# Kernel tuning notes

Hardware: AMD Instinct MI355X
Metric: run time of the kernel (lower is better)

The kernel has to match this reference:

```python
import math
import jax, jax.numpy as jnp
import numpy as np

D_MODEL = 256
N_HEADS = 8
D_K = D_MODEL // N_HEADS
BS = 2
SEQ = 2048
NEG = -1e32


def _linear(x, W, b):
    return x @ W + b


def _layernorm(x, g, b):
    m = jnp.mean(x, axis=-1, keepdims=True)
    v = jnp.mean((x - m) ** 2, axis=-1, keepdims=True)
    return (x - m) / jnp.sqrt(v + 1e-5) * g + b


def _attention(q, k, v, mask, gammas):
    # q,k,v: [b,h,s,dk]; mask: [1,1,s,s] bool; gammas: [h,1,1]
    d_k = q.shape[-1]
    scores = jnp.einsum('bhqd,bhkd->bhqk', q, k) / math.sqrt(d_k)
    S = scores.shape[-1]
    # distance-decay bias (computed under stop_gradient, as torch.no_grad + detach)
    sm = jax.lax.stop_gradient(jax.nn.softmax(jnp.where(mask, scores, NEG), axis=-1))
    distcum = jnp.cumsum(sm, axis=-1)
    disttot = jnp.sum(sm, axis=-1, keepdims=True)
    idx = jnp.arange(S, dtype=scores.dtype)
    pos = jnp.abs(idx[None, :] - idx[:, None])[None, None]  # |i-j|
    dist = jax.lax.stop_gradient(
        jnp.sqrt(jnp.clip((disttot - distcum) * pos, 0.0, None)))
    gamma = -jax.nn.softplus(gammas)[None]  # [1,h,1,1]
    eff = jnp.clip(jnp.exp(dist * gamma), 1e-5, 1e5)
    scores = jnp.where(mask, scores * eff, NEG)
    scores = jnp.where(mask, jax.nn.softmax(scores, axis=-1), 0.0)
    return jnp.einsum('bhqk,bhkd->bhqd', scores, v)


def _mha(qx, kx, vx, Wq, bq, Wk, bk, Wv, bv, Wo, bo, gammas, mask):
    bs = qx.shape[0]
    def split(x, W, b):
        return _linear(x, W, b).reshape(bs, -1, N_HEADS, D_K).transpose(0, 2, 1, 3)
    q = split(qx, Wq, bq)
    k = split(kx, Wk, bk)
    v = split(vx, Wv, bv)
    o = _attention(q, k, v, mask, gammas)
    o = o.transpose(0, 2, 1, 3).reshape(bs, -1, D_MODEL)
    return _linear(o, Wo, bo)


def _layer(query, key, values, Wq, bq, Wk, bk, Wv, bv, Wo, bo, gammas, ln_g, ln_b, peek_cur):
    S = query.shape[1]
    mask = jnp.tril(jnp.ones((S, S), dtype=bool), 0 if peek_cur else -1)[None, None]
    out = _mha(query, key, values, Wq, bq, Wk, bk, Wv, bv, Wo, bo, gammas, mask)
    return _layernorm(query + out, ln_g, ln_b)


def _forward(q_emb, qa_emb,
             b1_Wq, b1_bq, b1_Wv, b1_bv, b1_Wo, b1_bo, b1_gam, b1_lng, b1_lnb,
             b2_Wq, b2_bq, b2_Wv, b2_bv, b2_Wo, b2_bo, b2_gam, b2_lng, b2_lnb,
             b3_Wq, b3_bq, b3_Wk, b3_bk, b3_Wv, b3_bv, b3_Wo, b3_bo, b3_gam, b3_lng, b3_lnb,
             know_params, lk_W, lk_b, lv_W, lv_b):
    # blocks 1 & 2: kq_same -> k projection shares q projection weights
    hq = _layer(q_emb, q_emb, q_emb,
                b1_Wq, b1_bq, b1_Wq, b1_bq, b1_Wv, b1_bv, b1_Wo, b1_bo,
                b1_gam, b1_lng, b1_lnb, peek_cur=True)
    ha = _layer(qa_emb, qa_emb, qa_emb,
                b2_Wq, b2_bq, b2_Wq, b2_bq, b2_Wv, b2_bv, b2_Wo, b2_bo,
                b2_gam, b2_lng, b2_lnb, peek_cur=True)
    query = jnp.broadcast_to(know_params, hq.shape)
    h = _layer(query, hq, ha,
               b3_Wq, b3_bq, b3_Wk, b3_bk, b3_Wv, b3_bv, b3_Wo, b3_bo,
               b3_gam, b3_lng, b3_lnb, peek_cur=False)
    bs, S, d = hq.shape
    key = jax.nn.sigmoid(_linear(
        jnp.broadcast_to(know_params, (bs, S, d)).reshape(bs, S, N_HEADS, D_K),
        lk_W, lk_b)).reshape(bs * S, N_HEADS, d)
    value = jax.nn.sigmoid(_linear(
        h.reshape(bs, S, N_HEADS, D_K), lv_W, lv_b)).reshape(bs * S, N_HEADS, d)
    beta = jnp.einsum('nhd,nd->nh', key, q_emb.reshape(bs * S, d))
    alpha = jax.nn.softmax(beta, axis=-1)
    h = jnp.einsum('nh,nhd->nd', alpha, value).reshape(bs, S, d)
    return h


def setup_inputs() -> dict:
    keys = iter(jax.random.split(jax.random.key(0), 64))
    def nrm(shape, scale=0.02):
        return jax.random.normal(next(keys), shape, dtype=jnp.float32) * scale
    def uni(shape):
        return jax.random.uniform(next(keys), shape, dtype=jnp.float32, minval=-1.0, maxval=1.0)
    d = D_MODEL
    inp = {
        'q_emb': nrm((BS, SEQ, d), 1.0),
        'qa_emb': nrm((BS, SEQ, d), 1.0),
    }
    for blk in ('b1', 'b2'):
        inp[blk + '_Wq'] = nrm((d, d)); inp[blk + '_bq'] = jnp.zeros((d,), jnp.float32)
        inp[blk + '_Wv'] = nrm((d, d)); inp[blk + '_bv'] = jnp.zeros((d,), jnp.float32)
        inp[blk + '_Wo'] = nrm((d, d)); inp[blk + '_bo'] = jnp.zeros((d,), jnp.float32)
        inp[blk + '_gam'] = uni((N_HEADS, 1, 1))
        inp[blk + '_lng'] = jnp.ones((d,), jnp.float32)
        inp[blk + '_lnb'] = jnp.zeros((d,), jnp.float32)
    inp['b3_Wq'] = nrm((d, d)); inp['b3_bq'] = jnp.zeros((d,), jnp.float32)
    inp['b3_Wk'] = nrm((d, d)); inp['b3_bk'] = jnp.zeros((d,), jnp.float32)
    inp['b3_Wv'] = nrm((d, d)); inp['b3_bv'] = jnp.zeros((d,), jnp.float32)
    inp['b3_Wo'] = nrm((d, d)); inp['b3_bo'] = jnp.zeros((d,), jnp.float32)
    inp['b3_gam'] = uni((N_HEADS, 1, 1))
    inp['b3_lng'] = jnp.ones((d,), jnp.float32)
    inp['b3_lnb'] = jnp.zeros((d,), jnp.float32)
    inp['know_params'] = uni((1, 1, d))
    inp['lk_W'] = nrm((D_K, d)); inp['lk_b'] = jnp.zeros((d,), jnp.float32)
    inp['lv_W'] = nrm((D_K, d)); inp['lv_b'] = jnp.zeros((d,), jnp.float32)
    return inp


def reference(q_emb, qa_emb,
              b1_Wq, b1_bq, b1_Wv, b1_bv, b1_Wo, b1_bo, b1_gam, b1_lng, b1_lnb,
              b2_Wq, b2_bq, b2_Wv, b2_bv, b2_Wo, b2_bo, b2_gam, b2_lng, b2_lnb,
              b3_Wq, b3_bq, b3_Wk, b3_bk, b3_Wv, b3_bv, b3_Wo, b3_bo, b3_gam, b3_lng, b3_lnb,
              know_params, lk_W, lk_b, lv_W, lv_b):
    return _forward(q_emb, qa_emb,
                    b1_Wq, b1_bq, b1_Wv, b1_bv, b1_Wo, b1_bo, b1_gam, b1_lng, b1_lnb,
                    b2_Wq, b2_bq, b2_Wv, b2_bv, b2_Wo, b2_bo, b2_gam, b2_lng, b2_lnb,
                    b3_Wq, b3_bq, b3_Wk, b3_bk, b3_Wv, b3_bv, b3_Wo, b3_bo, b3_gam, b3_lng, b3_lnb,
                    know_params, lk_W, lk_b, lv_W, lv_b)
```

## Files before the change

### kernel.cpp

```cpp
#include <hip/hip_runtime.h>
#include <hip/hip_bf16.h>

#define DM 256
#define NH 8
#define DK 32
#define BSZ 2
#define SEQ 2048
#define ROWS (BSZ*SEQ)
#define RT 16
#define SRB 2312
#define SRBH 1144

static __device__ __forceinline__ int sw8(int j) { return j + ((j >> 6) << 3); }

typedef __attribute__((ext_vector_type(8))) short short8;
typedef __attribute__((ext_vector_type(4))) float f32x4;

static __device__ __forceinline__ unsigned short f2bf(float f) {
    unsigned u = __float_as_uint(f);
    return (unsigned short)((u + 0x7FFFu + ((u >> 16) & 1u)) >> 16);
}
static __device__ __forceinline__ float bf2f(unsigned short h) {
    return __uint_as_float(((unsigned)h) << 16);
}

static __device__ __forceinline__ unsigned cvtpk(float lo, float hi) {
    unsigned r;
    asm("v_cvt_pk_bf16_f32 %0, %1, %2" : "=v"(r) : "v"(lo), "v"(hi));
    return r;
}

static __device__ __forceinline__ float ex2(float x) { return __builtin_amdgcn_exp2f(x); }
static __device__ __forceinline__ float sqt(float x) { return __builtin_amdgcn_sqrtf(x); }
static __device__ __forceinline__ float rcp(float x) { return __builtin_amdgcn_rcpf(x); }

template<int CTRL, int RM>
static __device__ __forceinline__ float dppadd(float x) {
    int s = __builtin_amdgcn_update_dpp(0, __float_as_int(x), CTRL, RM, 0xf, true);
    return x + __int_as_float(s);
}
static __device__ __forceinline__ float scan32(float x) {
    x = dppadd<0x111, 0xf>(x);
    x = dppadd<0x112, 0xf>(x);
    x = dppadd<0x114, 0xf>(x);
    x = dppadd<0x118, 0xf>(x);
    x = dppadd<0x142, 0xa>(x);
    return x;
}
static __device__ __forceinline__ float red16(float x) {
    x = dppadd<0x0B1, 0xf>(x);
    x = dppadd<0x04E, 0xf>(x);
    x = dppadd<0x124, 0xf>(x);
    x = dppadd<0x128, 0xf>(x);
    return x;
}
static __device__ __forceinline__ float bcast31(float x) {
    return __int_as_float(__builtin_amdgcn_ds_swizzle(__float_as_int(x), 0x03E0));
}
static __device__ __forceinline__ float swz_x16(float x) {
    return __int_as_float(__builtin_amdgcn_ds_swizzle(__float_as_int(x), 0x401F));
}

static __device__ __forceinline__ void unpack4(uint2 u, float& s0, float& s1,
                                               float& s2, float& s3) {
    s0 = __uint_as_float(u.x << 16);
    s1 = __uint_as_float(u.x & 0xFFFF0000u);
    s2 = __uint_as_float(u.y << 16);
    s3 = __uint_as_float(u.y & 0xFFFF0000u);
}

static __device__ __forceinline__ uint2 decay_quad(
    float s0, float s1, float s2, float s3v,
    float e0, float e1, float e2, float e3,
    float cum, float pq, float linv,
    float l, float gamma2, float& l2)
{
    float p0, p1, p2, p3;
    cum += e0;
    { float dist = sqt(fmaxf((l - cum) * pq, 0.f));
      float eff = fmaxf(ex2(dist * gamma2), 1e-5f);
      p0 = ex2(s0 * eff); l2 += p0; }
    cum += e1;
    { float dist = sqt(fmaxf((l - cum) * (pq - linv), 0.f));
      float eff = fmaxf(ex2(dist * gamma2), 1e-5f);
      p1 = ex2(s1 * eff); l2 += p1; }
    cum += e2;
    { float dist = sqt(fmaxf((l - cum) * (pq - 2.f * linv), 0.f));
      float eff = fmaxf(ex2(dist * gamma2), 1e-5f);
      p2 = ex2(s2 * eff); l2 += p2; }
    cum += e3;
    { float dist = sqt(fmaxf((l - cum) * (pq - 3.f * linv), 0.f));
      float eff = fmaxf(ex2(dist * gamma2), 1e-5f);
      p3 = ex2(s3v * eff); l2 += p3; }
    uint2 st;
    st.x = cvtpk(p0, p1);
    st.y = cvtpk(p2, p3);
    return st;
}

#define MFMA_BF16 __builtin_amdgcn_mfma_f32_16x16x32_bf16
#define LOG2E 1.44269504088896340736f

static __device__ __forceinline__ float waveRedSum(float v) {
    #pragma unroll
    for (int off = 32; off > 0; off >>= 1) v += __shfl_down(v, off, 64);
    return v;
}

__global__ __launch_bounds__(256) void convert_w_kernel(
    const float* __restrict__ S0, const float* __restrict__ S1, const float* __restrict__ S2,
    const float* __restrict__ S3, const float* __restrict__ S4, const float* __restrict__ S5,
    const float* __restrict__ S6, const float* __restrict__ S7, const float* __restrict__ S8,
    unsigned short* __restrict__ dst,
    const float* __restrict__ know,
    const float* __restrict__ W3q, const float* __restrict__ b3q,
    const float* __restrict__ lkW, const float* __restrict__ lkb,
    float* __restrict__ q3row, float* __restrict__ key8)
{
    __shared__ float kn[DM];
    int s = blockIdx.y;
    if (s == 9) {
        if (blockIdx.x != 0) return;
        int t = threadIdx.x;
        kn[t] = know[t];
        __syncthreads();
        float acc = b3q[t];
        for (int c = 0; c < DM; ++c) acc += kn[c] * W3q[(size_t)c * DM + t];
        q3row[t] = acc;
        float bk = lkb[t];
        for (int h = 0; h < NH; ++h) {
            float a = bk;
            #pragma unroll
            for (int c = 0; c < DK; ++c) a += kn[h * DK + c] * lkW[(size_t)c * DM + t];
            key8[(size_t)h * DM + t] = 1.f / (1.f + __expf(-a));
        }
        return;
    }
    const float* W;
    if (s == 0) W = S0; else if (s == 1) W = S1; else if (s == 2) W = S2;
    else if (s == 3) W = S3; else if (s == 4) W = S4; else if (s == 5) W = S5;
    else if (s == 6) W = S6; else if (s == 7) W = S7; else W = S8;
    unsigned short* H = dst + (size_t)s * 131072;
    unsigned short* L = H + 65536;

    int e = blockIdx.x * 1024 + threadIdx.x * 4;
    int k = e >> 8, n = e & 255;
    float4 w4 = *(const float4*)(W + e);
    float v[4] = {w4.x, w4.y, w4.z, w4.w};
    #pragma unroll
    for (int i = 0; i < 4; ++i) {
        unsigned short h = f2bf(v[i]);
        H[(size_t)(n + i) * 256 + k] = h;
        L[(size_t)(n + i) * 256 + k] = (unsigned short)f2bf(v[i] - bf2f(h));
    }
}

__global__ __launch_bounds__(256) void gemm4_kernel(
    const float* __restrict__ X0, const unsigned short* __restrict__ H0, const float* __restrict__ B0,
    float* __restrict__ Y0, unsigned short* __restrict__ K0o, unsigned short* __restrict__ V0o,
    const float* __restrict__ X1, const unsigned short* __restrict__ H1, const float* __restrict__ B1,
    float* __restrict__ Y1, unsigned short* __restrict__ K1o, unsigned short* __restrict__ V1o,
    const float* __restrict__ X2, const unsigned short* __restrict__ H2, const float* __restrict__ B2,
    float* __restrict__ Y2, unsigned short* __restrict__ K2o, unsigned short* __restrict__ V2o,
    const float* __restrict__ X3, const unsigned short* __restrict__ H3, const float* __restrict__ B3,
    float* __restrict__ Y3, unsigned short* __restrict__ K3o, unsigned short* __restrict__ V3o)
{
    const float *X, *Bias; const unsigned short* H; float* Yf;
    unsigned short *KSo, *VSo;
    int s = blockIdx.y;
    if (s == 0)      { X = X0; H = H0; Bias = B0; Yf = Y0; KSo = K0o; VSo = V0o; }
    else if (s == 1) { X = X1; H = H1; Bias = B1; Yf = Y1; KSo = K1o; VSo = V1o; }
    else if (s == 2) { X = X2; H = H2; Bias = B2; Yf = Y2; KSo = K2o; VSo = V2o; }
    else             { X = X3; H = H3; Bias = B3; Yf = Y3; KSo = K3o; VSo = V3o; }
    const unsigned short* L = H + 65536;

    __shared__ __align__(16) unsigned short XhL[16 * 264];
    __shared__ __align__(16) unsigned short XlL[16 * 264];
    __shared__ __align__(16) unsigned short vt[256][24];
    int t = threadIdx.x;
    int r0 = blockIdx.x * 16;
    {
        int r = t >> 4, c0 = (t & 15) * 16;
        const float* xp = X + (size_t)(r0 + r) * DM + c0;
        #pragma unroll
        for (int i = 0; i < 16; i += 4) {
            float4 v4 = *(const float4*)(xp + i);
            float vv[4] = {v4.x, v4.y, v4.z, v4.w};
            #pragma unroll
            for (int j = 0; j < 4; ++j) {
                unsigned short h = f2bf(vv[j]);
                XhL[r * 264 + c0 + i + j] = h;
                XlL[r * 264 + c0 + i + j] = (unsigned short)f2bf(vv[j] - bf2f(h));
            }
        }
    }
    __syncthreads();
    int lane = t & 63, wv = t >> 6;
    int m = lane & 15, quad = lane >> 4;
    f32x4 aa[4];
    #pragma unroll
    for (int nt = 0; nt < 4; ++nt) { aa[nt][0]=0.f; aa[nt][1]=0.f; aa[nt][2]=0.f; aa[nt][3]=0.f; }
    #pragma unroll 1
    for (int kc = 0; kc < 8; ++kc) {
        int k0 = kc * 32;
        short8 Ah = *(const short8*)&XhL[m * 264 + k0 + quad * 8];
        short8 Al = *(const short8*)&XlL[m * 264 + k0 + quad * 8];
        size_t boff = (size_t)(wv * 64 + m) * 256 + k0 + quad * 8;
        #pragma unroll
        for (int nt = 0; nt < 4; ++nt) {
            short8 Bh = *(const short8*)(H + boff + nt * 16 * 256);
            short8 Bl = *(const short8*)(L + boff + nt * 16 * 256);
            aa[nt] = MFMA_BF16(Al, Bh, aa[nt], 0, 0, 0);
            aa[nt] = MFMA_BF16(Ah, Bl, aa[nt], 0, 0, 0);
            aa[nt] = MFMA_BF16(Ah, Bh, aa[nt], 0, 0, 0);
        }
    }
    int col0 = wv * 64 + m;
    #pragma unroll
    for (int nt = 0; nt < 4; ++nt) {
        int col = col0 + nt * 16;
        float bb = Bias[col];
        float yv[4];
        #pragma unroll
        for (int g = 0; g < 4; ++g) yv[g] = aa[nt][g] + bb;
        if (Yf) {
            #pragma unroll
            for (int g = 0; g < 4; ++g)
                Yf[(size_t)(r0 + quad * 4 + g) * DM + col] = yv[g];
        }
        if (KSo) {
            unsigned short* KH = KSo;
            unsigned short* KL = KSo + (size_t)ROWS * DM;
            #pragma unroll
            for (int g = 0; g < 4; ++g) {
                unsigned short hb = f2bf(yv[g]);
                KH[(size_t)(r0 + quad * 4 + g) * DM + col] = hb;
                KL[(size_t)(r0 + quad * 4 + g) * DM + col] =
                    (unsigned short)f2bf(yv[g] - bf2f(hb));
            }
        }
        if (VSo) {
            ushort4 h4;
            h4.x = f2bf(yv[0]); h4.y = f2bf(yv[1]);
            h4.z = f2bf(yv[2]); h4.w = f2bf(yv[3]);
            *(ushort4*)&vt[col][quad * 4] = h4;
        }
    }
    if (VSo) {
        __syncthreads();
        short8 v0 = *(const short8*)&vt[t][0];
        short8 v1 = *(const short8*)&vt[t][8];
        unsigned short* vp = VSo + (size_t)t * ROWS + r0;
        *(short8*)vp = v0;
        *(short8*)(vp + 8) = v1;
    }
}

__global__ __launch_bounds__(256) void gemm_ln2_kernel(
    const float* __restrict__ X0, const unsigned short* __restrict__ H0, const float* __restrict__ B0,
    const float* __restrict__ R0, const float* __restrict__ G0, const float* __restrict__ L0,
    float* __restrict__ Y0, int bc0,
    const float* __restrict__ X1, const unsigned short* __restrict__ H1, const float* __restrict__ B1,
    const float* __restrict__ R1, const float* __restrict__ G1, const float* __restrict__ L1,
    float* __restrict__ Y1, int bc1)
{
    const float *X, *Bias, *R, *G, *Lb; const unsigned short* H; float* Y; int bc;
    if (blockIdx.y == 0) { X=X0; H=H0; Bias=B0; R=R0; G=G0; Lb=L0; Y=Y0; bc=bc0; }
    else                 { X=X1; H=H1; Bias=B1; R=R1; G=G1; Lb=L1; Y=Y1; bc=bc1; }
    const unsigned short* L = H + 65536;

    __shared__ __align__(16) unsigned short XhL[16 * 264];
    __shared__ __align__(16) unsigned short XlL[16 * 264];
    __shared__ __align__(16) float yl[16 * 260];
    int t = threadIdx.x;
    int r0 = blockIdx.x * 16;
    {   int r = t >> 4, c0 = (t & 15) * 16;
        const float* xp = X + (size_t)(r0 + r) * DM + c0;
        #pragma unroll
        for (int i = 0; i < 16; i += 4) {
            float4 v4 = *(const float4*)(xp + i);
            float vv[4] = {v4.x, v4.y, v4.z, v4.w};
            #pragma unroll
            for (int j = 0; j < 4; ++j) {
                unsigned short h = f2bf(vv[j]);
                XhL[r * 264 + c0 + i + j] = h;
                XlL[r * 264 + c0 + i + j] = (unsigned short)f2bf(vv[j] - bf2f(h));
            }
        }
    }
    __syncthreads();
    int lane = t & 63, wv = t >> 6;
    int m = lane & 15, quad = lane >> 4;
    f32x4 aa[4];
    #pragma unroll
    for (int nt = 0; nt < 4; ++nt) { aa[nt][0]=0.f; aa[nt][1]=0.f; aa[nt][2]=0.f; aa[nt][3]=0.f; }
    #pragma unroll 1
    for (int kc = 0; kc < 8; ++kc) {
        int k0 = kc * 32;
        short8 Ah = *(const short8*)&XhL[m * 264 + k0 + quad * 8];
        short8 Al = *(const short8*)&XlL[m * 264 + k0 + quad * 8];
        size_t boff = (size_t)(wv * 64 + m) * 256 + k0 + quad * 8;
        #pragma unroll
        for (int nt = 0; nt < 4; ++nt) {
            short8 Bh = *(const short8*)(H + boff + nt * 16 * 256);
            short8 Bl = *(const short8*)(L + boff + nt * 16 * 256);
            aa[nt] = MFMA_BF16(Al, Bh, aa[nt], 0, 0, 0);
            aa[nt] = MFMA_BF16(Ah, Bl, aa[nt], 0, 0, 0);
            aa[nt] = MFMA_BF16(Ah, Bh, aa[nt], 0, 0, 0);
        }
    }
    {
        int col0 = wv * 64 + m;
        #pragma unroll
        for (int nt = 0; nt < 4; ++nt) {
            int col = col0 + nt * 16;
            float bb = Bias[col];
            #pragma unroll
            for (int g = 0; g < 4; ++g) {
                int row = quad * 4 + g;
                float res = bc ? R[col] : R[(size_t)(r0 + row) * DM + col];
                yl[row * 260 + col] = aa[nt][g] + bb + res;
            }
        }
    }
    __syncthreads();
    {
        int r = t >> 4, c0 = (t & 15) * 16;
        float vals[16];
        float part = 0.f;
        #pragma unroll
        for (int i = 0; i < 16; ++i) { vals[i] = yl[r * 260 + c0 + i]; part += vals[i]; }
        #pragma unroll
        for (int off = 8; off; off >>= 1) part += __shfl_xor(part, off, 16);
        float mean = part * (1.f / DM);
        float vp = 0.f;
        #pragma unroll
        for (int i = 0; i < 16; ++i) { float d = vals[i] - mean; vp += d * d; }
        #pragma unroll
        for (int off = 8; off; off >>= 1) vp += __shfl_xor(vp, off, 16);
        float rs = rsqrtf(vp * (1.f / DM) + 1e-5f);
        float* yp = Y + (size_t)(r0 + r) * DM + c0;
        #pragma unroll
        for (int i = 0; i < 16; i += 4) {
            float4 o;
            o.x = (vals[i+0] - mean) * rs * G[c0+i+0] + Lb[c0+i+0];
            o.y = (vals[i+1] - mean) * rs * G[c0+i+1] + Lb[c0+i+1];
            o.z = (vals[i+2] - mean) * rs * G[c0+i+2] + Lb[c0+i+2];
            o.w = (vals[i+3] - mean) * rs * G[c0+i+3] + Lb[c0+i+3];
            *(float4*)(yp + i) = o;
        }
    }
}

__global__ __launch_bounds__(256) void score3a_kernel(
    const float* __restrict__ q3row, const float* __restrict__ K3,
    unsigned short* __restrict__ S3, float* __restrict__ C3,
    float* __restrict__ Csum)
{
    __shared__ float wsum[4];
    int s = blockIdx.x;
    int bh = blockIdx.y;
    int b = bh >> 3, h = bh & 7;
    int t = threadIdx.x;
    int lane = t & 63, wv = t >> 6;
    int j = s * 256 + t;
    const float scaleL2 = 0.17677669529663687f * LOG2E;
    float qv[DK];
    #pragma unroll
    for (int d = 0; d < DK; d += 4) {
        float4 qq = *(const float4*)(q3row + h * DK + d);
        qv[d+0] = qq.x * scaleL2; qv[d+1] = qq.y * scaleL2;
        qv[d+2] = qq.z * scaleL2; qv[d+3] = qq.w * scaleL2;
    }
    const float* kp = K3 + ((size_t)b * SEQ + j) * DM + h * DK;
    float kv[DK];
    #pragma unroll
    for (int d = 0; d < DK; d += 4) {
        float4 kq = *(const float4*)(kp + d);
        kv[d+0] = kq.x; kv[d+1] = kq.y; kv[d+2] = kq.z; kv[d+3] = kq.w;
    }
    float sc = 0.f;
    #pragma unroll
    for (int d = 0; d < DK; ++d) sc += qv[d] * kv[d];
    unsigned short sb16 = f2bf(sc);
    float e = ex2(bf2f(sb16));
    float x = e;
    #pragma unroll
    for (int off = 1; off < 64; off <<= 1) {
        float y = __shfl_up(x, off, 64);
        if (lane >= off) x += y;
    }
    if (lane == 63) wsum[wv] = x;
    __syncthreads();
    float woff = 0.f;
    for (int w = 0; w < wv; ++w) woff += wsum[w];
    float inc = woff + x;
    S3[(size_t)bh * SEQ + j] = sb16;
    C3[(size_t)bh * SEQ + j] = inc;
    if (t == 255) Csum[bh * 8 + s] = inc;
}

__global__ __launch_bounds__(256) void score3b_kernel(
    const float* __restrict__ Csum, float* __restrict__ C3)
{
    int s = blockIdx.x + 1;
    int bh = blockIdx.y;
    int t = threadIdx.x;
    float off = 0.f;
    for (int w = 0; w < s; ++w) off += Csum[bh * 8 + w];
    C3[(size_t)bh * SEQ + s * 256 + t] += off;
}

__global__ __launch_bounds__(512) void attn12_kernel(
    const float* __restrict__ Q0,
    const unsigned short* __restrict__ KS0, const unsigned short* __restrict__ VS0,
    const float* __restrict__ g0, float* __restrict__ O0,
    const float* __restrict__ Q1,
    const unsigned short* __restrict__ KS1, const unsigned short* __restrict__ VS1,
    const float* __restrict__ g1, float* __restrict__ O1)
{
    __shared__ __align__(16) unsigned short SB[RT * SRB];
    __shared__ float qs[RT][DK];
    __shared__ float l2inv_s[RT];
    __shared__ float rowsum[8 * RT];

    int bx, by;
    {
        int flat = (int)blockIdx.y * 128 + (int)blockIdx.x;
        int per = (32 * 128) >> 3;
        int nf = (flat & 7) * per + (flat >> 3);
        by = nf >> 7;
        bx = nf & 127;
    }
    int set = by >> 4, bh = by & 15;
    const float* Q = set ? Q1 : Q0;
    const unsigned short* KS = set ? KS1 : KS0;
    const unsigned short* VS = set ? VS1 : VS0;
    const float* gm = set ? g1 : g0;
    float* O = set ? O1 : O0;

    int b = bh >> 3, h = bh & 7;
    int i0 = (127 - bx) * RT;
    int t = threadIdx.x;
    size_t base = ((size_t)b * SEQ) * DM + (size_t)h * DK;

    int njAll = i0 + RT;
    int njPad32 = (njAll + 31) & ~31;
    int njPad128 = (njAll + 127) & ~127;
    const float scaleL2 = 0.17677669529663687f * LOG2E;

    {
        int r = t >> 5, d = t & 31;
        qs[r][d] = Q[base + (size_t)(i0 + r) * DM + d];
    }
    __syncthreads();

    {
        int wave = t >> 6, lane = t & 63;
        int m = lane & 15, quad = lane >> 4;

        float av[8];
        {
            float4 qa = *(const float4*)&qs[m][8 * quad];
            float4 qb = *(const float4*)&qs[m][8 * quad + 4];
            av[0]=qa.x*scaleL2; av[1]=qa.y*scaleL2; av[2]=qa.z*scaleL2; av[3]=qa.w*scaleL2;
            av[4]=qb.x*scaleL2; av[5]=qb.y*scaleL2; av[6]=qb.z*scaleL2; av[7]=qb.w*scaleL2;
        }
        short8 Ah;
        #pragma unroll
        for (int i = 0; i < 8; ++i) Ah[i] = (short)f2bf(av[i]);

        const unsigned short* KH = KS;
        const unsigned short* KL = KS + (size_t)ROWS * DM;
        size_t rowb = (size_t)b * SEQ;
        int njr0 = i0 + quad * 4 + 1;
        float rp0 = 0.f, rp1 = 0.f, rp2 = 0.f, rp3 = 0.f;
        int nChunks = (njAll + 15) >> 4;
        #pragma unroll 2
        for (int c = wave; c < nChunks; c += 8) {
            int j0 = c << 4;
            size_t off = (rowb + j0 + m) * DM + h * DK + quad * 8;
            short8 Bh = *(const short8*)&KH[off];
            short8 Bl = *(const short8*)&KL[off];
            f32x4 acc = {0.f, 0.f, 0.f, 0.f};
            acc = MFMA_BF16(Ah, Bl, acc, 0, 0, 0);
            acc = MFMA_BF16(Ah, Bh, acc, 0, 0, 0);
            int jcol = j0 + m;
            int sj = sw8(jcol);
            unsigned pk01 = cvtpk(acc[0], acc[1]);
            unsigned pk23 = cvtpk(acc[2], acc[3]);
            SB[(quad * 4 + 0) * SRB + sj] = (unsigned short)pk01;
            SB[(quad * 4 + 1) * SRB + sj] = (unsigned short)(pk01 >> 16);
            SB[(quad * 4 + 2) * SRB + sj] = (unsigned short)pk23;
            SB[(quad * 4 + 3) * SRB + sj] = (unsigned short)(pk23 >> 16);
            rp0 += (jcol < njr0 + 0) ? ex2(acc[0]) : 0.f;
            rp1 += (jcol < njr0 + 1) ? ex2(acc[1]) : 0.f;
            rp2 += (jcol < njr0 + 2) ? ex2(acc[2]) : 0.f;
            rp3 += (jcol < njr0 + 3) ? ex2(acc[3]) : 0.f;
        }
        rp0 = red16(rp0); rp1 = red16(rp1);
        rp2 = red16(rp2); rp3 = red16(rp3);
        if (m == 0) {
            rowsum[wave * RT + quad * 4 + 0] = rp0;
            rowsum[wave * RT + quad * 4 + 1] = rp1;
            rowsum[wave * RT + quad * 4 + 2] = rp2;
            rowsum[wave * RT + quad * 4 + 3] = rp3;
        }
    }
    __syncthreads();

    {
        int r = t >> 5, c = t & 31;
        int nj = i0 + r + 1;
        for (int j = nj + c; j < njPad128; j += 32)
            SB[r * SRB + sw8(j)] = 0xFF80u;
    }
    __syncthreads();

    {
        int r = t >> 5, c = t & 31;
        int i = i0 + r;
        unsigned short* Sr = SB + r * SRB;
        float gamma2 = -log1pf(__expf(gm[h])) * LOG2E;

        float l = 0.f;
        #pragma unroll
        for (int w = 0; w < 8; ++w) l += rowsum[w * RT + r];
        float linv = rcp(l);

        float l2 = 0.f;
        float Bc = 0.f;
        int nIter = (njPad32 + 127) >> 7;
        int pairs = nIter >> 1;
        uint2 nxA, nxB;
        nxA = *(const uint2*)&Sr[sw8(4 * c)];
        nxB = *(const uint2*)&Sr[sw8(4 * c + 128)];
        #pragma unroll 1
        for (int k = 0; k < pairs; ++k) {
            int j4a = 256 * k + 4 * c;
            int j4b = j4a + 128;
            uint2 uA = nxA;
            uint2 uB = nxB;
            nxA = *(const uint2*)&Sr[sw8(j4a + 256)];
            nxB = *(const uint2*)&Sr[sw8(j4b + 256)];
            float a0, a1, a2, a3, b0, b1, b2, b3;
            unpack4(uA, a0, a1, a2, a3);
            unpack4(uB, b0, b1, b2, b3);
            float eA0 = ex2(a0), eA1 = ex2(a1), eA2 = ex2(a2), eA3 = ex2(a3);
            float eB0 = ex2(b0), eB1 = ex2(b1), eB2 = ex2(b2), eB3 = ex2(b3);
            float sigA = eA0 + eA1 + eA2 + eA3;
            float sigB = eB0 + eB1 + eB2 + eB3;
            float xA = scan32(sigA);
            float xB = scan32(sigB);
            float totA = bcast31(xA);
            float totB = bcast31(xB);
            float cumA = Bc + (xA - sigA);
            float cumB = Bc + totA + (xB - sigB);
            Bc += totA + totB;
            float pqA = (float)(i - j4a) * linv;
            float pqB = pqA - 128.f * linv;
            uint2 stA = decay_quad(a0, a1, a2, a3, eA0, eA1, eA2, eA3,
                                   cumA, pqA, linv, l, gamma2, l2);
            uint2 stB = decay_quad(b0, b1, b2, b3, eB0, eB1, eB2, eB3,
                                   cumB, pqB, linv, l, gamma2, l2);
            *(uint2*)&Sr[sw8(j4a)] = stA;
            *(uint2*)&Sr[sw8(j4b)] = stB;
        }
        if (nIter & 1) {
            int j4a = 256 * pairs + 4 * c;
            uint2 uA = nxA;
            float a0, a1, a2, a3;
            unpack4(uA, a0, a1, a2, a3);
            float eA0 = ex2(a0), eA1 = ex2(a1), eA2 = ex2(a2), eA3 = ex2(a3);
            float sigA = eA0 + eA1 + eA2 + eA3;
            float xA = scan32(sigA);
            float cumA = Bc + (xA - sigA);
            float pqA = (float)(i - j4a) * linv;
            uint2 stA = decay_quad(a0, a1, a2, a3, eA0, eA1, eA2, eA3,
                                   cumA, pqA, linv, l, gamma2, l2);
            *(uint2*)&Sr[sw8(j4a)] = stA;
        }
        l2 = red16(l2);
        l2 += swz_x16(l2);
        if (c == 0) l2inv_s[r] = rcp(l2);
    }
    __syncthreads();

    {
        int wave = t >> 6, lane = t & 63;
        int n16 = lane & 15, quad = lane >> 4;
        const unsigned short* VH = VS;
        size_t vb0 = (size_t)(h * DK + n16) * ROWS + (size_t)b * SEQ;
        size_t vb1 = (size_t)(h * DK + 16 + n16) * ROWS + (size_t)b * SEQ;
        f32x4 oc0 = {0.f,0.f,0.f,0.f}, oc1 = {0.f,0.f,0.f,0.f};
        #pragma unroll 2
        for (int j0 = wave * 32; j0 < njPad32; j0 += 256) {
            short8 Ap = *(const short8*)&SB[n16 * SRB + sw8(j0 + quad * 8)];
            int jo = j0 + quad * 8;
            short8 Bh0 = *(const short8*)&VH[vb0 + jo];
            short8 Bh1 = *(const short8*)&VH[vb1 + jo];
            oc0 = MFMA_BF16(Ap, Bh0, oc0, 0, 0, 0);
            oc1 = MFMA_BF16(Ap, Bh1, oc1, 0, 0, 0);
        }
        __syncthreads();
        float* FS = (float*)SB;
        #pragma unroll
        for (int g = 0; g < 4; ++g) {
            int row = quad * 4 + g;
            FS[wave * 512 + row * 32 + n16] = oc0[g];
            FS[wave * 512 + row * 32 + 16 + n16] = oc1[g];
        }
    }
    __syncthreads();
    {
        float* FS = (float*)SB;
        int r2 = t >> 5, d = t & 31;
        float sum = 0.f;
        #pragma unroll
        for (int w = 0; w < 8; ++w)
            sum += FS[w * 512 + r2 * 32 + d];
        O[base + (size_t)(i0 + r2) * DM + d] = sum * l2inv_s[r2];
    }
}

__global__ __launch_bounds__(512) void attn3_kernel(
    const unsigned short* __restrict__ VS, const float* __restrict__ gm8,
    float* __restrict__ O,
    const unsigned short* __restrict__ S3g, const float* __restrict__ C3g)
{
    __shared__ __align__(16) unsigned short SBH[RT * SRBH];
    __shared__ float l2inv_s[RT];

    int bx, by;
    {
        int flat = (int)blockIdx.y * 128 + (int)blockIdx.x;
        int per = (16 * 128) >> 3;
        int nf = (flat & 7) * per + (flat >> 3);
        by = nf >> 7;
        bx = nf & 127;
    }
    int bh = by;
    int b = bh >> 3, h = bh & 7;
    int i0 = (127 - bx) * RT;
    int t = threadIdx.x;
    size_t base = ((size_t)b * SEQ) * DM + (size_t)h * DK;

    int njAll = i0 + RT - 1;
    int njPad32 = (njAll + 31) & ~31;
    int E = ((njPad32 + 127) >> 7) << 7;

    int r = t >> 5, c = t & 31;
    int i = i0 + r;
    int nj = i;
    unsigned short* Sr = SBH + r * SRBH;
    float gamma2 = -log1pf(__expf(gm8[h])) * LOG2E;
    const unsigned short* s3p = S3g + (size_t)bh * SEQ;
    const float* c3p = C3g + (size_t)bh * SEQ;
    float Lc = (nj > 0) ? c3p[nj - 1] : 0.f;
    float linv = (nj > 0) ? rcp(Lc) : 0.f;
    float li2 = linv + linv, li3 = li2 + linv;
    float l2 = 0.f;

    int wave = t >> 6, lane = t & 63;
    int n16 = lane & 15, quad = lane >> 4;
    size_t rowb = (size_t)b * SEQ;
    size_t vb0 = (size_t)(h * DK + n16) * ROWS + rowb;
    size_t vb1 = (size_t)(h * DK + 16 + n16) * ROWS + rowb;
    f32x4 oc0 = {0.f,0.f,0.f,0.f}, oc1 = {0.f,0.f,0.f,0.f};

    #pragma unroll 1
    for (int hbase = 0; hbase < E; hbase += 1024) {
        int hend = min(hbase + 1024, E);
        #pragma unroll 1
        for (int j4 = hbase + 4 * c; j4 < hend; j4 += 128) {
            uint2 su = *(const uint2*)&s3p[j4];
            float4 C4 = *(const float4*)&c3p[j4];
            float s0 = __uint_as_float(su.x << 16);
            float s1 = __uint_as_float(su.x & 0xFFFF0000u);
            float s2 = __uint_as_float(su.y << 16);
            float s3v = __uint_as_float(su.y & 0xFFFF0000u);
            float pq = (float)(i - j4) * linv;
            float p0, p1, p2, p3;
            { float dist = sqt(fmaxf((Lc - C4.x) * pq, 0.f));
              float eff = fmaxf(ex2(dist * gamma2), 1e-5f);
              p0 = (j4 + 0 < nj) ? ex2(s0 * eff) : 0.f; l2 += p0; }
            { float dist = sqt(fmaxf((Lc - C4.y) * (pq - linv), 0.f));
              float eff = fmaxf(ex2(dist * gamma2), 1e-5f);
              p1 = (j4 + 1 < nj) ? ex2(s1 * eff) : 0.f; l2 += p1; }
            { float dist = sqt(fmaxf((Lc - C4.z) * (pq - li2), 0.f));
              float eff = fmaxf(ex2(dist * gamma2), 1e-5f);
              p2 = (j4 + 2 < nj) ? ex2(s2 * eff) : 0.f; l2 += p2; }
            { float dist = sqt(fmaxf((Lc - C4.w) * (pq - li3), 0.f));
              float eff = fmaxf(ex2(dist * gamma2), 1e-5f);
              p3 = (j4 + 3 < nj) ? ex2(s3v * eff) : 0.f; l2 += p3; }
            uint2 st;
            st.x = cvtpk(p0, p1);
            st.y = cvtpk(p2, p3);
            *(uint2*)&Sr[sw8(j4 - hbase)] = st;
        }
        __syncthreads();
        int pend = min(hbase + 1024, njPad32);
        #pragma unroll 1
        for (int j0 = hbase + wave * 32; j0 < pend; j0 += 256) {
            short8 Ap = *(const short8*)&SBH[n16 * SRBH + sw8(j0 - hbase + quad * 8)];
            int jo = j0 + quad * 8;
            short8 Bh0 = *(const short8*)&VS[vb0 + jo];
            short8 Bh1 = *(const short8*)&VS[vb1 + jo];
            oc0 = MFMA_BF16(Ap, Bh0, oc0, 0, 0, 0);
            oc1 = MFMA_BF16(Ap, Bh1, oc1, 0, 0, 0);
        }
        __syncthreads();
    }

    l2 = red16(l2);
    l2 += swz_x16(l2);
    if (c == 0) l2inv_s[r] = (nj > 0) ? rcp(l2) : 0.f;
    float* FS = (float*)SBH;
    #pragma unroll
    for (int g = 0; g < 4; ++g) {
        int row = quad * 4 + g;
        FS[wave * 512 + row * 32 + n16] = oc0[g];
        FS[wave * 512 + row * 32 + 16 + n16] = oc1[g];
    }
    __syncthreads();
    {
        int r2 = t >> 5, d = t & 31;
        float sum = 0.f;
        #pragma unroll
        for (int w = 0; w < 8; ++w)
            sum += FS[w * 512 + r2 * 32 + d];
        O[base + (size_t)(i0 + r2) * DM + d] = sum * l2inv_s[r2];
    }
}

__global__ __launch_bounds__(256) void readout_kernel(
    const float* __restrict__ h3, const float* __restrict__ qe,
    const float* __restrict__ key8,
    const float* __restrict__ lvW, const float* __restrict__ lvb,
    float* __restrict__ out)
{
    __shared__ float hrow[DM], qrow[DM];
    __shared__ float red8[4][NH];
    int n = blockIdx.x, t = threadIdx.x;
    int lane = t & 63, wid = t >> 6;
    hrow[t] = h3[(size_t)n * DM + t];
    qrow[t] = qe[(size_t)n * DM + t];
    __syncthreads();
    float ph[NH];
    #pragma unroll
    for (int h = 0; h < NH; ++h) {
        float v = key8[(size_t)h * DM + t] * qrow[t];
        v = waveRedSum(v);
        ph[h] = v;
    }
    if (lane == 0) {
        #pragma unroll
        for (int h = 0; h < NH; ++h) red8[wid][h] = ph[h];
    }
    __syncthreads();
    float beta[NH];
    #pragma unroll
    for (int h = 0; h < NH; ++h)
        beta[h] = red8[0][h] + red8[1][h] + red8[2][h] + red8[3][h];
    float bv = lvb[t];
    float vh[NH];
    for (int h = 0; h < NH; ++h) {
        float a = bv;
        #pragma unroll
        for (int c = 0; c < DK; ++c) a += hrow[h * DK + c] * lvW[(size_t)c * DM + t];
        vh[h] = 1.f / (1.f + __expf(-a));
    }
    float mb = beta[0];
    #pragma unroll
    for (int h = 1; h < NH; ++h) mb = fmaxf(mb, beta[h]);
    float se = 0.f, eh[NH];
    #pragma unroll
    for (int h = 0; h < NH; ++h) { eh[h] = __expf(beta[h] - mb); se += eh[h]; }
    float sinv = 1.f / se;
    float o = 0.f;
    #pragma unroll
    for (int h = 0; h < NH; ++h) o += eh[h] * sinv * vh[h];
    out[(size_t)n * DM + t] = o;
}

extern "C" void kernel_launch(void* const* d_in, const int* in_sizes, int n_in,
                              void* d_out, int out_size, void* d_ws, size_t ws_size,
                              hipStream_t stream) {
    (void)in_sizes; (void)n_in; (void)out_size; (void)ws_size;
    const float* q_emb  = (const float*)d_in[0];
    const float* qa_emb = (const float*)d_in[1];
    const float* b1_Wq = (const float*)d_in[2];
    const float* b1_bq = (const float*)d_in[3];
    const float* b1_Wv = (const float*)d_in[4];
    const float* b1_bv = (const float*)d_in[5];
    const float* b1_Wo = (const float*)d_in[6];
    const float* b1_bo = (const float*)d_in[7];
    const float* b1_gam = (const float*)d_in[8];
    const float* b1_lng = (const float*)d_in[9];
    const float* b1_lnb = (const float*)d_in[10];
    const float* b2_Wq = (const float*)d_in[11];
    const float* b2_bq = (const float*)d_in[12];
    const float* b2_Wv = (const float*)d_in[13];
    const float* b2_bv = (const float*)d_in[14];
    const float* b2_Wo = (const float*)d_in[15];
    const float* b2_bo = (const float*)d_in[16];
    const float* b2_gam = (const float*)d_in[17];
    const float* b2_lng = (const float*)d_in[18];
    const float* b2_lnb = (const float*)d_in[19];
    const float* b3_Wq = (const float*)d_in[20];
    const float* b3_bq = (const float*)d_in[21];
    const float* b3_Wk = (const float*)d_in[22];
    const float* b3_bk = (const float*)d_in[23];
    const float* b3_Wv = (const float*)d_in[24];
    const float* b3_bv = (const float*)d_in[25];
    const float* b3_Wo = (const float*)d_in[26];
    const float* b3_bo = (const float*)d_in[27];
    const float* b3_gam = (const float*)d_in[28];
    const float* b3_lng = (const float*)d_in[29];
    const float* b3_lnb = (const float*)d_in[30];
    const float* know  = (const float*)d_in[31];
    const float* lk_W  = (const float*)d_in[32];
    const float* lk_b  = (const float*)d_in[33];
    const float* lv_W  = (const float*)d_in[34];
    const float* lv_b  = (const float*)d_in[35];

    const size_t SLAB = (size_t)ROWS * DM;
    const size_t USLAB = 2 * SLAB;
    float* A1 = (float*)d_ws;
    float* A2 = A1 + SLAB;
    float* C1 = A2 + SLAB;
    float* C2 = C1 + SLAB;
    unsigned short* KS1 = (unsigned short*)(C2 + SLAB);
    unsigned short* KS2 = KS1 + USLAB;
    unsigned short* VS1 = KS2 + USLAB;
    unsigned short* VS2 = VS1 + USLAB;
    float* q3row = (float*)(VS2 + USLAB);
    float* key8  = q3row + DM;
    unsigned short* Wsp = (unsigned short*)(key8 + NH * DM);
    unsigned short* S3buf = Wsp + (size_t)9 * 131072;
    float* C3buf = (float*)(S3buf + 16 * SEQ);
    float* Csum  = C3buf + 16 * SEQ;
    float* hq = (float*)KS1;
    float* ha = (float*)KS2;
    float* k3 = A1;
    unsigned short* VS3 = VS1;
    float* O3 = C1;
    float* h3 = C2;

    auto WH = [&](int i) { return Wsp + (size_t)i * 131072; };

    dim3 blk(256);
    dim3 ablk(512);
    dim3 agrid2(SEQ / RT, 32);
    dim3 agrid1(SEQ / RT, 16);
    dim3 rgrid(ROWS);

    convert_w_kernel<<<dim3(64, 10), blk, 0, stream>>>(
        b1_Wq, b1_Wv, b1_Wo, b2_Wq, b2_Wv, b2_Wo, b3_Wk, b3_Wv, b3_Wo, Wsp,
        know, b3_Wq, b3_bq, lk_W, lk_b, q3row, key8);

    gemm4_kernel<<<dim3(ROWS/16, 4), blk, 0, stream>>>(
        q_emb,  WH(0), b1_bq, A1,      KS1,     nullptr,
        q_emb,  WH(1), b1_bv, nullptr, nullptr, VS1,
        qa_emb, WH(3), b2_bq, A2,      KS2,     nullptr,
        qa_emb, WH(4), b2_bv, nullptr, nullptr, VS2);

    attn12_kernel<<<agrid2, ablk, 0, stream>>>(
        A1, KS1, VS1, b1_gam, C1,
        A2, KS2, VS2, b2_gam, C2);

    gemm_ln2_kernel<<<dim3(ROWS/16, 2), blk, 0, stream>>>(
        C1, WH(2), b1_bo, q_emb,  b1_lng, b1_lnb, hq, 0,
        C2, WH(5), b2_bo, qa_emb, b2_lng, b2_lnb, ha, 0);

    gemm4_kernel<<<dim3(ROWS/16, 2), blk, 0, stream>>>(
        hq, WH(6), b3_bk, k3,      nullptr, nullptr,
        ha, WH(7), b3_bv, nullptr, nullptr, VS3,
        hq, WH(6), b3_bk, k3,      nullptr, nullptr,
        hq, WH(6), b3_bk, k3,      nullptr, nullptr);

    score3a_kernel<<<dim3(8, 16), blk, 0, stream>>>(q3row, k3, S3buf, C3buf, Csum);
    score3b_kernel<<<dim3(7, 16), blk, 0, stream>>>(Csum, C3buf);

    attn3_kernel<<<agrid1, ablk, 0, stream>>>(VS3, b3_gam, O3, S3buf, C3buf);

    gemm_ln2_kernel<<<dim3(ROWS/16, 1), blk, 0, stream>>>(
        O3, WH(8), b3_bo, know, b3_lng, b3_lnb, h3, 1,
        O3, WH(8), b3_bo, know, b3_lng, b3_lnb, h3, 1);

    readout_kernel<<<rgrid, blk, 0, stream>>>(h3, q_emb, key8, lv_W, lv_b,
                                              (float*)d_out);
}
```

Baseline: 425.3 us.

## Keep attention scores in registers and compute decay per chunk in attn12

Restructures the attn12 kernel so each wave keeps its bf16 QK scores in registers instead of writing them all to shared memory. Per-32-column block exp-sums are stored in a small LDS table and prefix-scanned, and each wave then computes the distance-decay probabilities for its own chunks with an in-wave 16-lane scan. The probabilities are written to a half-size LDS buffer in two 1024-column phases and fed straight into the PV MFMA. This cuts shared-memory footprint and LDS round-trips and removes the separate per-row scan pass, at the cost of many more live registers (32 packed score registers per thread) and extra barriers.

Result: slower. 440.8 us (+3.6%).

```diff
diff --git a/kernel.cpp b/kernel.cpp
--- a/kernel.cpp
+++ b/kernel.cpp
@@ -8,8 +8,8 @@
 #define SEQ 2048
 #define ROWS (BSZ*SEQ)
 #define RT 16
-#define SRB 2312
 #define SRBH 1144
+#define SRBW 1160
 
 static __device__ __forceinline__ int sw8(int j) { return j + ((j >> 6) << 3); }
 
@@ -47,6 +47,13 @@
     x = dppadd<0x142, 0xa>(x);
     return x;
 }
+static __device__ __forceinline__ float scan16(float x) {
+    x = dppadd<0x111, 0xf>(x);
+    x = dppadd<0x112, 0xf>(x);
+    x = dppadd<0x114, 0xf>(x);
+    x = dppadd<0x118, 0xf>(x);
+    return x;
+}
 static __device__ __forceinline__ float red16(float x) {
     x = dppadd<0x0B1, 0xf>(x);
     x = dppadd<0x04E, 0xf>(x);
@@ -57,45 +64,11 @@
 static __device__ __forceinline__ float bcast31(float x) {
     return __int_as_float(__builtin_amdgcn_ds_swizzle(__float_as_int(x), 0x03E0));
 }
+static __device__ __forceinline__ float bcast15(float x) {
+    return __int_as_float(__builtin_amdgcn_ds_swizzle(__float_as_int(x), 0x01F0));
+}
 static __device__ __forceinline__ float swz_x16(float x) {
     return __int_as_float(__builtin_amdgcn_ds_swizzle(__float_as_int(x), 0x401F));
-}
-
-static __device__ __forceinline__ void unpack4(uint2 u, float& s0, float& s1,
-                                               float& s2, float& s3) {
-    s0 = __uint_as_float(u.x << 16);
-    s1 = __uint_as_float(u.x & 0xFFFF0000u);
-    s2 = __uint_as_float(u.y << 16);
-    s3 = __uint_as_float(u.y & 0xFFFF0000u);
-}
-
-static __device__ __forceinline__ uint2 decay_quad(
-    float s0, float s1, float s2, float s3v,
-    float e0, float e1, float e2, float e3,
-    float cum, float pq, float linv,
-    float l, float gamma2, float& l2)
-{
-    float p0, p1, p2, p3;
-    cum += e0;
-    { float dist = sqt(fmaxf((l - cum) * pq, 0.f));
-      float eff = fmaxf(ex2(dist * gamma2), 1e-5f);
-      p0 = ex2(s0 * eff); l2 += p0; }
-    cum += e1;
-    { float dist = sqt(fmaxf((l - cum) * (pq - linv), 0.f));
-      float eff = fmaxf(ex2(dist * gamma2), 1e-5f);
-      p1 = ex2(s1 * eff); l2 += p1; }
-    cum += e2;
-    { float dist = sqt(fmaxf((l - cum) * (pq - 2.f * linv), 0.f));
-      float eff = fmaxf(ex2(dist * gamma2), 1e-5f);
-      p2 = ex2(s2 * eff); l2 += p2; }
-    cum += e3;
-    { float dist = sqt(fmaxf((l - cum) * (pq - 3.f * linv), 0.f));
-      float eff = fmaxf(ex2(dist * gamma2), 1e-5f);
-      p3 = ex2(s3v * eff); l2 += p3; }
-    uint2 st;
-    st.x = cvtpk(p0, p1);
-    st.y = cvtpk(p2, p3);
-    return st;
 }
 
 #define MFMA_BF16 __builtin_amdgcn_mfma_f32_16x16x32_bf16
@@ -419,10 +392,10 @@
     const unsigned short* __restrict__ KS1, const unsigned short* __restrict__ VS1,
     const float* __restrict__ g1, float* __restrict__ O1)
 {
-    __shared__ __align__(16) unsigned short SB[RT * SRB];
-    __shared__ float qs[RT][DK];
-    __shared__ float l2inv_s[RT];
-    __shared__ float rowsum[8 * RT];
+    __shared__ __align__(16) unsigned short PB[RT * SRBW];
+    __shared__ float ct[16 * 64];
+    __shared__ float l_s[16];
+    __shared__ float wl2[8][16];
 
     int bx, by;
     {
@@ -442,184 +415,194 @@
     int b = bh >> 3, h = bh & 7;
     int i0 = (127 - bx) * RT;
     int t = threadIdx.x;
+    int wave = t >> 6, lane = t & 63;
+    int m = lane & 15, quad = lane >> 4;
     size_t base = ((size_t)b * SEQ) * DM + (size_t)h * DK;
+    size_t rowb = (size_t)b * SEQ;
 
     int njAll = i0 + RT;
-    int njPad32 = (njAll + 31) & ~31;
-    int njPad128 = (njAll + 127) & ~127;
+    int nChunks = njAll >> 4;
+    int nb32 = (nChunks + 1) >> 1;
+    int njPad32 = nb32 << 5;
+
     const float scaleL2 = 0.17677669529663687f * LOG2E;
 
+    short8 Ah;
     {
-        int r = t >> 5, d = t & 31;
-        qs[r][d] = Q[base + (size_t)(i0 + r) * DM + d];
+        const float* qp = Q + base + (size_t)(i0 + m) * DM + quad * 8;
+        float4 qa = *(const float4*)qp;
+        float4 qb = *(const float4*)(qp + 4);
+        float av[8] = {qa.x, qa.y, qa.z, qa.w, qb.x, qb.y, qb.z, qb.w};
+        #pragma unroll
+        for (int i = 0; i < 8; ++i) Ah[i] = (short)f2bf(av[i] * scaleL2);
+    }
+
+    const unsigned short* KH = KS;
+    const unsigned short* KL = KS + (size_t)ROWS * DM;
+    int njr[4];
+    #pragma unroll
+    for (int g = 0; g < 4; ++g) njr[g] = i0 + quad * 4 + g + 1;
+
+    unsigned spk[32];
+
+    #pragma unroll
+    for (int bb = 0; bb < 8; ++bb) {
+        int blk = wave + bb * 8;
+        if (blk < nb32) {
+            float ctv[4] = {0.f, 0.f, 0.f, 0.f};
+            #pragma unroll
+            for (int half = 0; half < 2; ++half) {
+                int c = blk * 2 + half;
+                if (c < nChunks) {
+                    int j0 = c << 4;
+                    size_t off = (rowb + j0 + m) * DM + h * DK + quad * 8;
+                    short8 Bh = *(const short8*)&KH[off];
+                    short8 Bl = *(const short8*)&KL[off];
+                    f32x4 acc = {0.f, 0.f, 0.f, 0.f};
+                    acc = MFMA_BF16(Ah, Bl, acc, 0, 0, 0);
+                    acc = MFMA_BF16(Ah, Bh, acc, 0, 0, 0);
+                    int jcol = j0 + m;
+                    unsigned short u0 = f2bf(acc[0]), u1 = f2bf(acc[1]);
+                    unsigned short u2 = f2bf(acc[2]), u3 = f2bf(acc[3]);
+                    spk[bb * 4 + half * 2 + 0] = (unsigned)u0 | ((unsigned)u1 << 16);
+                    spk[bb * 4 + half * 2 + 1] = (unsigned)u2 | ((unsigned)u3 << 16);
+                    ctv[0] += (jcol < njr[0]) ? ex2(bf2f(u0)) : 0.f;
+                    ctv[1] += (jcol < njr[1]) ? ex2(bf2f(u1)) : 0.f;
+                    ctv[2] += (jcol < njr[2]) ? ex2(bf2f(u2)) : 0.f;
+                    ctv[3] += (jcol < njr[3]) ? ex2(bf2f(u3)) : 0.f;
+                }
+            }
+            #pragma unroll
+            for (int g = 0; g < 4; ++g) ctv[g] = red16(ctv[g]);
+            if (m == 0) {
+                #pragma unroll
+                for (int g = 0; g < 4; ++g) ct[(quad * 4 + g) * 64 + blk] = ctv[g];
+            }
+        }
     }
     __syncthreads();
 
     {
-        int wave = t >> 6, lane = t & 63;
-        int m = lane & 15, quad = lane >> 4;
-
-        float av[8];
-        {
-            float4 qa = *(const float4*)&qs[m][8 * quad];
-            float4 qb = *(const float4*)&qs[m][8 * quad + 4];
-            av[0]=qa.x*scaleL2; av[1]=qa.y*scaleL2; av[2]=qa.z*scaleL2; av[3]=qa.w*scaleL2;
-            av[4]=qb.x*scaleL2; av[5]=qb.y*scaleL2; av[6]=qb.z*scaleL2; av[7]=qb.w*scaleL2;
-        }
-        short8 Ah;
-        #pragma unroll
-        for (int i = 0; i < 8; ++i) Ah[i] = (short)f2bf(av[i]);
-
-        const unsigned short* KH = KS;
-        const unsigned short* KL = KS + (size_t)ROWS * DM;
-        size_t rowb = (size_t)b * SEQ;
-        int njr0 = i0 + quad * 4 + 1;
-        float rp0 = 0.f, rp1 = 0.f, rp2 = 0.f, rp3 = 0.f;
-        int nChunks = (njAll + 15) >> 4;
-        #pragma unroll 2
-        for (int c = wave; c < nChunks; c += 8) {
-            int j0 = c << 4;
-            size_t off = (rowb + j0 + m) * DM + h * DK + quad * 8;
-            short8 Bh = *(const short8*)&KH[off];
-            short8 Bl = *(const short8*)&KL[off];
-            f32x4 acc = {0.f, 0.f, 0.f, 0.f};
-            acc = MFMA_BF16(Ah, Bl, acc, 0, 0, 0);
-            acc = MFMA_BF16(Ah, Bh, acc, 0, 0, 0);
-            int jcol = j0 + m;
-            int sj = sw8(jcol);
-            unsigned pk01 = cvtpk(acc[0], acc[1]);
-            unsigned pk23 = cvtpk(acc[2], acc[3]);
-            SB[(quad * 4 + 0) * SRB + sj] = (unsigned short)pk01;
-            SB[(quad * 4 + 1) * SRB + sj] = (unsigned short)(pk01 >> 16);
-            SB[(quad * 4 + 2) * SRB + sj] = (unsigned short)pk23;
-            SB[(quad * 4 + 3) * SRB + sj] = (unsigned short)(pk23 >> 16);
-            rp0 += (jcol < njr0 + 0) ? ex2(acc[0]) : 0.f;
-            rp1 += (jcol < njr0 + 1) ? ex2(acc[1]) : 0.f;
-            rp2 += (jcol < njr0 + 2) ? ex2(acc[2]) : 0.f;
-            rp3 += (jcol < njr0 + 3) ? ex2(acc[3]) : 0.f;
-        }
-        rp0 = red16(rp0); rp1 = red16(rp1);
-        rp2 = red16(rp2); rp3 = red16(rp3);
-        if (m == 0) {
-            rowsum[wave * RT + quad * 4 + 0] = rp0;
-            rowsum[wave * RT + quad * 4 + 1] = rp1;
-            rowsum[wave * RT + quad * 4 + 2] = rp2;
-            rowsum[wave * RT + quad * 4 + 3] = rp3;
-        }
-    }
-    __syncthreads();
-
+        int r = t >> 5, c0 = t & 31;
+        float v0 = (2 * c0     < nb32) ? ct[r * 64 + 2 * c0]     : 0.f;
+        float v1 = (2 * c0 + 1 < nb32) ? ct[r * 64 + 2 * c0 + 1] : 0.f;
+        float loc = v0 + v1;
+        float x = scan32(loc);
+        float tot = bcast31(x);
+        float excl = x - loc;
+        float2 pr; pr.x = excl; pr.y = excl + v0;
+        *(float2*)&ct[r * 64 + 2 * c0] = pr;
+        if (c0 == 0) l_s[r] = tot;
+    }
+    __syncthreads();
+
+    float gamma2 = -log1pf(__expf(gm[h])) * LOG2E;
+    float linv[4], rowc[4], l2[4];
+    #pragma unroll
+    for (int g = 0; g < 4; ++g) {
+        linv[g] = rcp(l_s[quad * 4 + g]);
+        rowc[g] = (float)(i0 + quad * 4 + g - m);
+        l2[g] = 0.f;
+    }
+
+    size_t vb0 = (size_t)(h * DK + m) * ROWS + rowb;
+    size_t vb1 = vb0 + (size_t)16 * ROWS;
+    f32x4 oc0 = {0.f,0.f,0.f,0.f}, oc1 = {0.f,0.f,0.f,0.f};
+
+    #pragma unroll
+    for (int q = 0; q < 2; ++q) {
+        if (q * 1024 < njPad32) {
+            #pragma unroll
+            for (int j = 0; j < 4; ++j) {
+                int bb = q * 4 + j;
+                int blk = wave + bb * 8;
+                if (blk < nb32) {
+                    float pre[4];
+                    #pragma unroll
+                    for (int g = 0; g < 4; ++g) pre[g] = ct[(quad * 4 + g) * 64 + blk];
+                    #pragma unroll
+                    for (int half = 0; half < 2; ++half) {
+                        int c = blk * 2 + half;
+                        int j0 = c << 4;
+                        int lc0 = j0 - q * 1024;
+                        int sbase = lc0 + ((lc0 >> 6) << 3);
+                        unsigned short* Srow = PB + sbase + m;
+                        if (c < nChunks) {
+                            int jcol = j0 + m;
+                            unsigned pk0 = spk[bb * 4 + half * 2 + 0];
+                            unsigned pk1 = spk[bb * 4 + half * 2 + 1];
+                            float s[4];
+                            s[0] = bf2f((unsigned short)pk0);
+                            s[1] = bf2f((unsigned short)(pk0 >> 16));
+                            s[2] = bf2f((unsigned short)pk1);
+                            s[3] = bf2f((unsigned short)(pk1 >> 16));
+                            float x[4];
+                            #pragma unroll
+                            for (int g = 0; g < 4; ++g)
+                                x[g] = (jcol < njr[g]) ? ex2(s[g]) : 0.f;
+                            #pragma unroll
+                            for (int g = 0; g < 4; ++g) x[g] = scan16(x[g]);
+                            #pragma unroll
+                            for (int g = 0; g < 4; ++g) {
+                                float cum = pre[g] + x[g];
+                                float pbv = rowc[g] - (float)j0;
+                                float d2 = fmaxf((1.f - cum * linv[g]) * pbv, 0.f);
+                                float eff = fmaxf(ex2(sqt(d2) * gamma2), 1e-5f);
+                                float p = (jcol < njr[g]) ? ex2(s[g] * eff) : 0.f;
+                                l2[g] += p;
+                                Srow[(quad * 4 + g) * SRBW] = f2bf(p);
+                            }
+                            if (half == 0) {
+                                #pragma unroll
+                                for (int g = 0; g < 4; ++g) pre[g] += bcast15(x[g]);
+                            }
+                        } else {
+                            #pragma unroll
+                            for (int g = 0; g < 4; ++g)
+                                Srow[(quad * 4 + g) * SRBW] = 0;
+                        }
+                    }
+                }
+            }
+            __syncthreads();
+            int pend = min((q + 1) * 1024, njPad32);
+            #pragma unroll 1
+            for (int j0 = q * 1024 + wave * 32; j0 < pend; j0 += 256) {
+                int lj = j0 - q * 1024 + quad * 8;
+                short8 Ap = *(const short8*)&PB[m * SRBW + lj + ((lj >> 6) << 3)];
+                int jo = j0 + quad * 8;
+                short8 Bh0 = *(const short8*)&VS[vb0 + jo];
+                short8 Bh1 = *(const short8*)&VS[vb1 + jo];
+                oc0 = MFMA_BF16(Ap, Bh0, oc0, 0, 0, 0);
+                oc1 = MFMA_BF16(Ap, Bh1, oc1, 0, 0, 0);
+            }
+            __syncthreads();
+        }
+    }
+
+    #pragma unroll
+    for (int g = 0; g < 4; ++g) l2[g] = red16(l2[g]);
+    if (m == 0) {
+        #pragma unroll
+        for (int g = 0; g < 4; ++g) wl2[wave][quad * 4 + g] = l2[g];
+    }
+    float* FS = (float*)PB;
+    #pragma unroll
+    for (int g = 0; g < 4; ++g) {
+        int row = quad * 4 + g;
+        FS[wave * 512 + row * 32 + m] = oc0[g];
+        FS[wave * 512 + row * 32 + 16 + m] = oc1[g];
+    }
+    __syncthreads();
     {
-        int r = t >> 5, c = t & 31;
-        int nj = i0 + r + 1;
-        for (int j = nj + c; j < njPad128; j += 32)
-            SB[r * SRB + sw8(j)] = 0xFF80u;
-    }
-    __syncthreads();
-
-    {
-        int r = t >> 5, c = t & 31;
-        int i = i0 + r;
-        unsigned short* Sr = SB + r * SRB;
-        float gamma2 = -log1pf(__expf(gm[h])) * LOG2E;
-
-        float l = 0.f;
-        #pragma unroll
-        for (int w = 0; w < 8; ++w) l += rowsum[w * RT + r];
-        float linv = rcp(l);
-
-        float l2 = 0.f;
-        float Bc = 0.f;
-        int nIter = (njPad32 + 127) >> 7;
-        int pairs = nIter >> 1;
-        uint2 nxA, nxB;
-        nxA = *(const uint2*)&Sr[sw8(4 * c)];
-        nxB = *(const uint2*)&Sr[sw8(4 * c + 128)];
-        #pragma unroll 1
-        for (int k = 0; k < pairs; ++k) {
-            int j4a = 256 * k + 4 * c;
-            int j4b = j4a + 128;
-            uint2 uA = nxA;
-            uint2 uB = nxB;
-            nxA = *(const uint2*)&Sr[sw8(j4a + 256)];
-            nxB = *(const uint2*)&Sr[sw8(j4b + 256)];
-            float a0, a1, a2, a3, b0, b1, b2, b3;
-            unpack4(uA, a0, a1, a2, a3);
-            unpack4(uB, b0, b1, b2, b3);
-            float eA0 = ex2(a0), eA1 = ex2(a1), eA2 = ex2(a2), eA3 = ex2(a3);
-            float eB0 = ex2(b0), eB1 = ex2(b1), eB2 = ex2(b2), eB3 = ex2(b3);
-            float sigA = eA0 + eA1 + eA2 + eA3;
-            float sigB = eB0 + eB1 + eB2 + eB3;
-            float xA = scan32(sigA);
-            float xB = scan32(sigB);
-            float totA = bcast31(xA);
-            float totB = bcast31(xB);
-            float cumA = Bc + (xA - sigA);
-            float cumB = Bc + totA + (xB - sigB);
-            Bc += totA + totB;
-            float pqA = (float)(i - j4a) * linv;
-            float pqB = pqA - 128.f * linv;
-            uint2 stA = decay_quad(a0, a1, a2, a3, eA0, eA1, eA2, eA3,
-                                   cumA, pqA, linv, l, gamma2, l2);
-            uint2 stB = decay_quad(b0, b1, b2, b3, eB0, eB1, eB2, eB3,
-                                   cumB, pqB, linv, l, gamma2, l2);
-            *(uint2*)&Sr[sw8(j4a)] = stA;
-            *(uint2*)&Sr[sw8(j4b)] = stB;
-        }
-        if (nIter & 1) {
-            int j4a = 256 * pairs + 4 * c;
-            uint2 uA = nxA;
-            float a0, a1, a2, a3;
-            unpack4(uA, a0, a1, a2, a3);
-            float eA0 = ex2(a0), eA1 = ex2(a1), eA2 = ex2(a2), eA3 = ex2(a3);
-            float sigA = eA0 + eA1 + eA2 + eA3;
-            float xA = scan32(sigA);
-            float cumA = Bc + (xA - sigA);
-            float pqA = (float)(i - j4a) * linv;
-            uint2 stA = decay_quad(a0, a1, a2, a3, eA0, eA1, eA2, eA3,
-                                   cumA, pqA, linv, l, gamma2, l2);
-            *(uint2*)&Sr[sw8(j4a)] = stA;
-        }
-        l2 = red16(l2);
-        l2 += swz_x16(l2);
-        if (c == 0) l2inv_s[r] = rcp(l2);
-    }
-    __syncthreads();
-
-    {
-        int wave = t >> 6, lane = t & 63;
-        int n16 = lane & 15, quad = lane >> 4;
-        const unsigned short* VH = VS;
-        size_t vb0 = (size_t)(h * DK + n16) * ROWS + (size_t)b * SEQ;
-        size_t vb1 = (size_t)(h * DK + 16 + n16) * ROWS + (size_t)b * SEQ;
-        f32x4 oc0 = {0.f,0.f,0.f,0.f}, oc1 = {0.f,0.f,0.f,0.f};
-        #pragma unroll 2
-        for (int j0 = wave * 32; j0 < njPad32; j0 += 256) {
-            short8 Ap = *(const short8*)&SB[n16 * SRB + sw8(j0 + quad * 8)];
-            int jo = j0 + quad * 8;
-            short8 Bh0 = *(const short8*)&VH[vb0 + jo];
-            short8 Bh1 = *(const short8*)&VH[vb1 + jo];
-            oc0 = MFMA_BF16(Ap, Bh0, oc0, 0, 0, 0);
-            oc1 = MFMA_BF16(Ap, Bh1, oc1, 0, 0, 0);
-        }
-        __syncthreads();
-        float* FS = (float*)SB;
-        #pragma unroll
-        for (int g = 0; g < 4; ++g) {
-            int row = quad * 4 + g;
-            FS[wave * 512 + row * 32 + n16] = oc0[g];
-            FS[wave * 512 + row * 32 + 16 + n16] = oc1[g];
-        }
-    }
-    __syncthreads();
-    {
-        float* FS = (float*)SB;
         int r2 = t >> 5, d = t & 31;
-        float sum = 0.f;
-        #pragma unroll
-        for (int w = 0; w < 8; ++w)
+        float sum = 0.f, lt = 0.f;
+        #pragma unroll
+        for (int w = 0; w < 8; ++w) {
             sum += FS[w * 512 + r2 * 32 + d];
-        O[base + (size_t)(i0 + r2) * DM + d] = sum * l2inv_s[r2];
+            lt += wl2[w][r2];
+        }
+        O[base + (size_t)(i0 + r2) * DM + d] = sum * rcp(lt);
     }
 }
 
```
